# Performance work log

Measured on AMD Instinct MI355X. Metric: run time of the kernel, lower is better.

Reference implementation:

```python
import jax, jax.numpy as jnp
import numpy as np

EPS = 1e-6
STRIDE = 2  # kv_pool_stride
NUM_HEADS = 8

def _layernorm(x, w, b):
    mu = jnp.mean(x, axis=-1, keepdims=True)
    var = jnp.mean(jnp.square(x - mu), axis=-1, keepdims=True)
    return (x - mu) * jax.lax.rsqrt(var + EPS) * w + b

def setup_inputs() -> dict:
    key = jax.random.key(0)
    B, H, W, C = 8, 56, 56, 384
    hidden = int(C * 2.0)
    ks = jax.random.split(key, 12)
    s = 0.02
    return {
        "x": jax.random.normal(ks[0], (B, H * W, C), jnp.float32),
        "ln1_w": jnp.ones((C,), jnp.float32),
        "ln1_b": jnp.zeros((C,), jnp.float32),
        "qw": jax.random.normal(ks[1], (C, C), jnp.float32) * s,
        "qb": jnp.zeros((C,), jnp.float32),
        "kw": jax.random.normal(ks[2], (C, C), jnp.float32) * s,
        "kb": jnp.zeros((C,), jnp.float32),
        "vw": jax.random.normal(ks[3], (C, C), jnp.float32) * s,
        "vb": jnp.zeros((C,), jnp.float32),
        "pw": jax.random.normal(ks[4], (C, C), jnp.float32) * s,
        "pb": jnp.zeros((C,), jnp.float32),
        "ln2_w": jnp.ones((C,), jnp.float32),
        "ln2_b": jnp.zeros((C,), jnp.float32),
        "fc1_w": jax.random.normal(ks[5], (C, hidden), jnp.float32) * s,
        "fc1_b": jnp.zeros((hidden,), jnp.float32),
        "fc2_w": jax.random.normal(ks[6], (hidden, C), jnp.float32) * s,
        "fc2_b": jnp.zeros((C,), jnp.float32),
        "H": 56,
        "W": 56,
    }

def reference(x, ln1_w, ln1_b, qw, qb, kw, kb, vw, vb, pw, pb,
              ln2_w, ln2_b, fc1_w, fc1_b, fc2_w, fc2_b, H, W):
    B, N, C = x.shape
    h = NUM_HEADS
    d = C // h
    scale = d ** -0.5

    # Attention branch: Q from norm1(x); K,V from RAW x (as in source), KV avg-pooled 2x2
    q_tok = _layernorm(x, ln1_w, ln1_b)
    s = STRIDE
    Hk, Wk = H // s, W // s
    kv = x.reshape(B, Hk, s, Wk, s, C).mean(axis=(2, 4)).reshape(B, Hk * Wk, C)

    q = (q_tok @ qw + qb).reshape(B, N, h, d)
    k = (kv @ kw + kb).reshape(B, Hk * Wk, h, d)
    v = (kv @ vw + vb).reshape(B, Hk * Wk, h, d)

    attn = jnp.einsum('bqhd,bkhd->bhqk', q, k) * scale
    attn = jax.nn.softmax(attn, axis=-1)
    out = jnp.einsum('bhqk,bkhd->bqhd', attn, v).reshape(B, N, C)
    x = x + (out @ pw + pb)

    # MLP branch (GELU exact, matching torch nn.GELU default)
    y = _layernorm(x, ln2_w, ln2_b)
    y = jax.nn.gelu(y @ fc1_w + fc1_b, approximate=False)
    x = x + (y @ fc2_w + fc2_b)
    return x
```

## Files before the change

kernel.cpp:

```cpp
#include <hip/hip_runtime.h>
#include <math.h>

#define B_    8
#define N_TOK 3136
#define C_    384
#define DH    48
#define NK    784
#define HID   768
#define M1    25088
#define M2    6272
#define M1Q   6272

typedef unsigned short u16;
typedef __attribute__((ext_vector_type(8))) short bf16x8;
typedef __attribute__((ext_vector_type(4))) float f32x4;

__device__ __forceinline__ float b2f(u16 u) {
  return __uint_as_float(((unsigned)u) << 16);
}
__device__ __forceinline__ u16 f2b(float f) {
  unsigned u = __float_as_uint(f);
  return (u16)((u + 0x7fffu + ((u >> 16) & 1u)) >> 16);
}
__device__ __forceinline__ void gload_lds16(const u16* g, u16* l) {
  __builtin_amdgcn_global_load_lds(
      (const __attribute__((address_space(1))) void*)g,
      (__attribute__((address_space(3))) void*)l, 16, 0, 0);
}
__device__ __forceinline__ unsigned cvtpk_bf16(float a, float b) {
  unsigned r;
  asm("v_cvt_pk_bf16_f32 %0, %1, %2" : "=v"(r) : "v"(a), "v"(b));
  return r;
}
__device__ __forceinline__ float exp2_fast(float x) {
  float r;
  asm("v_exp_f32 %0, %1" : "=v"(r) : "v"(x));
  return r;
}

__global__ __launch_bounds__(256) void ln1_pool(
    const float* __restrict__ X, const float* __restrict__ w,
    const float* __restrict__ b, u16* __restrict__ Y, u16* __restrict__ KV) {
  if (blockIdx.x < M1 / 4) {
    const int row = blockIdx.x * 4 + (threadIdx.x >> 6);
    const int lane = threadIdx.x & 63;
    const size_t base = (size_t)row * C_;
    float v[6];
#pragma unroll
    for (int i = 0; i < 6; ++i) v[i] = X[base + lane + 64 * i];
    float s = 0.f;
#pragma unroll
    for (int i = 0; i < 6; ++i) s += v[i];
#pragma unroll
    for (int off = 32; off > 0; off >>= 1) s += __shfl_xor(s, off);
    const float mu = s * (1.0f / C_);
    float q = 0.f;
#pragma unroll
    for (int i = 0; i < 6; ++i) { float d = v[i] - mu; q += d * d; }
#pragma unroll
    for (int off = 32; off > 0; off >>= 1) q += __shfl_xor(q, off);
    const float r = rsqrtf(q * (1.0f / C_) + 1e-6f);
#pragma unroll
    for (int i = 0; i < 6; ++i) {
      int c = lane + 64 * i;
      Y[base + c] = f2b((v[i] - mu) * r * w[c] + b[c]);
    }
  } else {
    int t = (blockIdx.x - M1 / 4) * 256 + threadIdx.x;
    if (t >= M2 * C_) return;
    int c = t % C_;
    int row = t / C_;
    int bb = row / NK;
    int rr = row - bb * NK;
    int hk = rr / 28;
    int wk = rr - hk * 28;
    const float* p = X + ((size_t)(bb * N_TOK + hk * 112 + wk * 2)) * C_ + c;
    KV[t] = f2b(0.25f * (p[0] + p[C_] + p[56 * C_] + p[57 * C_]));
  }
}

__global__ __launch_bounds__(256) void ln2_rows(const u16* __restrict__ X,
    const float* __restrict__ w, const float* __restrict__ b, u16* __restrict__ Y) {
  const int row = blockIdx.x * 4 + (threadIdx.x >> 6);
  const int lane = threadIdx.x & 63;
  const size_t base = (size_t)row * C_;
  float v[6];
#pragma unroll
  for (int i = 0; i < 6; ++i) v[i] = b2f(X[base + lane + 64 * i]);
  float s = 0.f;
#pragma unroll
  for (int i = 0; i < 6; ++i) s += v[i];
#pragma unroll
  for (int off = 32; off > 0; off >>= 1) s += __shfl_xor(s, off);
  const float mu = s * (1.0f / C_);
  float q = 0.f;
#pragma unroll
  for (int i = 0; i < 6; ++i) { float d = v[i] - mu; q += d * d; }
#pragma unroll
  for (int off = 32; off > 0; off >>= 1) q += __shfl_xor(q, off);
  const float r = rsqrtf(q * (1.0f / C_) + 1e-6f);
#pragma unroll
  for (int i = 0; i < 6; ++i) {
    int c = lane + 64 * i;
    Y[base + c] = f2b((v[i] - mu) * r * w[c] + b[c]);
  }
}

struct TransArgs {
  const float* src[6];
  u16* dst[6];
  int K[6], N[6], tx[6], ty[6];
};
__global__ __launch_bounds__(256) void transpose_all(TransArgs a) {
  const int id = blockIdx.z;
  if ((int)blockIdx.x >= a.tx[id] || (int)blockIdx.y >= a.ty[id]) return;
  const float* W = a.src[id];
  u16* WT = a.dst[id];
  const int K = a.K[id], N = a.N[id];
  __shared__ u16 tile[64][73];
  const int k0 = blockIdx.y * 64, n0 = blockIdx.x * 64;
  for (int i = threadIdx.x; i < 64 * 64; i += 256) {
    int kk = i >> 6, nn = i & 63;
    tile[kk][nn] = f2b(W[(size_t)(k0 + kk) * N + n0 + nn]);
  }
  __syncthreads();
  for (int i = threadIdx.x; i < 64 * 64; i += 256) {
    int nn = i >> 6, kk = i & 63;
    WT[(size_t)(n0 + nn) * K + k0 + kk] = tile[kk][nn];
  }
}

template<int EPI, bool RES32, bool OUT32>
__device__ __forceinline__ void gemm_core(
    const u16* __restrict__ A, const u16* __restrict__ BT,
    const float* __restrict__ bias, const void* __restrict__ resv,
    void* __restrict__ Cv, int N, int K, float oscale, int m0, int n0) {
  __shared__ u16 As[128 * 64];
  __shared__ u16 Bs[128 * 64];
  const int tid  = threadIdx.x;
  const int wave = tid >> 6;
  const int lane = tid & 63;
  const int quad = lane >> 4;
  const int ll   = lane & 15;
  const int wm   = wave >> 1, wn = wave & 1;

  const int srow = wave * 32 + (lane >> 3);
  const int sgs  = lane & 7;

  f32x4 acc[4][4];
#pragma unroll
  for (int i = 0; i < 4; ++i)
#pragma unroll
    for (int j = 0; j < 4; ++j) acc[i][j] = (f32x4){0.f, 0.f, 0.f, 0.f};

  for (int kk0 = 0; kk0 < K; kk0 += 64) {
    __syncthreads();
#pragma unroll
    for (int c = 0; c < 4; ++c) {
      const int r = srow + c * 8;
      const int g = sgs ^ (r & 7);
      gload_lds16(A  + (size_t)(m0 + r) * K + kk0 + g * 8,
                  As + (size_t)(wave * 32 + c * 8) * 64);
      gload_lds16(BT + (size_t)(n0 + r) * K + kk0 + g * 8,
                  Bs + (size_t)(wave * 32 + c * 8) * 64);
    }
    __syncthreads();
#pragma unroll
    for (int ks = 0; ks < 2; ++ks) {
      const int gsw = (quad + 4 * ks) ^ (ll & 7);
      bf16x8 af[4], bfr[4];
#pragma unroll
      for (int im = 0; im < 4; ++im)
        af[im] = *(const bf16x8*)&As[(size_t)(wm * 64 + im * 16 + ll) * 64 + gsw * 8];
#pragma unroll
      for (int jn = 0; jn < 4; ++jn)
        bfr[jn] = *(const bf16x8*)&Bs[(size_t)(wn * 64 + jn * 16 + ll) * 64 + gsw * 8];
#pragma unroll
      for (int im = 0; im < 4; ++im)
#pragma unroll
        for (int jn = 0; jn < 4; ++jn)
          acc[im][jn] = __builtin_amdgcn_mfma_f32_16x16x32_bf16(
              af[im], bfr[jn], acc[im][jn], 0, 0, 0);
    }
  }

  float bb[4];
#pragma unroll
  for (int jn = 0; jn < 4; ++jn) bb[jn] = bias[n0 + wn * 64 + jn * 16 + ll];
#pragma unroll
  for (int im = 0; im < 4; ++im) {
    const int row = m0 + wm * 64 + im * 16 + quad * 4;
#pragma unroll
    for (int jn = 0; jn < 4; ++jn) {
      const int col = n0 + wn * 64 + jn * 16 + ll;
#pragma unroll
      for (int r = 0; r < 4; ++r) {
        float o = (acc[im][jn][r] + bb[jn]) * oscale;
        if (EPI == 1) {
          o = 0.5f * o * (1.0f + erff(o * 0.70710678118654752f));
        } else if (EPI == 2) {
          size_t ri = (size_t)(row + r) * N + col;
          o += RES32 ? ((const float*)resv)[ri] : b2f(((const u16*)resv)[ri]);
        }
        if (OUT32) ((float*)Cv)[(size_t)(row + r) * N + col] = o;
        else       ((u16*)Cv)[(size_t)(row + r) * N + col] = f2b(o);
      }
    }
  }
}

template<int EPI, bool RES32, bool OUT32>
__global__ __launch_bounds__(256) void gemm_bt(
    const u16* __restrict__ A, const u16* __restrict__ BT,
    const float* __restrict__ bias, const void* __restrict__ resv,
    void* __restrict__ Cv, int N, int K) {
  gemm_core<EPI, RES32, OUT32>(A, BT, bias, resv, Cv, N, K, 1.0f,
                               blockIdx.y << 7, blockIdx.x << 7);
}

struct QKVArgs {
  const u16* A[3];
  const u16* BT[3];
  const float* bias[3];
  u16* C[3];
  int M[3];
  float osc[3];
};
__global__ __launch_bounds__(256) void gemm_qkv(QKVArgs a) {
  const int z = blockIdx.z;
  const int m0 = blockIdx.y << 7;
  if (m0 >= a.M[z]) return;
  gemm_core<0, false, false>(a.A[z], a.BT[z], a.bias[z], nullptr, a.C[z],
                             C_, C_, a.osc[z], m0, blockIdx.x << 7);
}

#define QS_STR 72
__global__ __launch_bounds__(512) void attn_mfma(
    const u16* __restrict__ Q, const u16* __restrict__ Kb,
    const u16* __restrict__ Vb, u16* __restrict__ O) {
  __shared__ u16 Ks[2][64 * 64];
  __shared__ u16 Vt[2][48 * QS_STR];
  const int tid  = threadIdx.x;
  const int wave = tid >> 6;
  const int lane = tid & 63;
  const int quad = lane >> 4;
  const int ll   = lane & 15;
  const int blk  = blockIdx.x;
  const int orig = (blk & 7) * 200 + (blk >> 3);
  const int bh   = orig / 25;
  const int qt   = orig - bh * 25;
  const int b    = bh >> 3, h = bh & 7;
  const int q0   = qt * 128;

  bf16x8 qf0, qf1;
  {
    int qrow = q0 + wave * 16 + ll;
    if (qrow >= N_TOK) qrow = N_TOK - 1;
    const u16* qp = Q + ((size_t)(b * N_TOK) + qrow) * C_ + h * DH;
    qf0 = *(const bf16x8*)(qp + quad * 8);
    if (quad < 2) qf1 = *(const bf16x8*)(qp + 32 + quad * 8);
    else          qf1 = (bf16x8){0, 0, 0, 0, 0, 0, 0, 0};
  }

  const int krow = (wave << 3) + (lane >> 3);
  const int kgrp = (lane & 7) ^ (lane >> 3);
  const size_t kbase_g = (size_t)(b * NK) * C_ + h * DH + kgrp * 8;

  uint4 vreg;
  const int vkey  = lane;
  const int vcol  = ((vkey >> 5) << 5) + (((vkey & 15) >> 2) << 3) +
                    (((vkey >> 4) & 1) << 2) + (vkey & 3);

  {
    int kk = krow; if (kk >= NK) kk = NK - 1;
    gload_lds16(Kb + kbase_g + (size_t)kk * C_, &Ks[0][wave << 9]);
    if (wave < 6) {
      int vk = vkey; if (vk >= NK) vk = NK - 1;
      vreg = *(const uint4*)(Vb + ((size_t)(b * NK) + vk) * C_ + h * DH + wave * 8);
      const u16* vp = (const u16*)&vreg;
#pragma unroll
      for (int j = 0; j < 8; ++j)
        Vt[0][(wave * 8 + j) * QS_STR + vcol] = vp[j];
    }
  }
  __syncthreads();

  f32x4 Ofr[3] = {{0.f,0.f,0.f,0.f},{0.f,0.f,0.f,0.f},{0.f,0.f,0.f,0.f}};
  f32x4 Sden = {0.f, 0.f, 0.f, 0.f};
  const short oneb = (short)0x3F80;
  const bf16x8 ones = {oneb, oneb, oneb, oneb, oneb, oneb, oneb, oneb};

  for (int t = 0; t < 13; ++t) {
    const int cur = t & 1, nxt = cur ^ 1;

    if (t < 12) {
      const int knext = (t + 1) * 64;
      int kk = knext + krow; if (kk >= NK) kk = NK - 1;
      gload_lds16(Kb + kbase_g + (size_t)kk * C_, &Ks[nxt][wave << 9]);
      if (wave < 6) {
        int vk = knext + vkey; if (vk >= NK) vk = NK - 1;
        vreg = *(const uint4*)(Vb + ((size_t)(b * NK) + vk) * C_ + h * DH + wave * 8);
      }
    }

    f32x4 S[4];
    __builtin_amdgcn_s_setprio(1);
#pragma unroll
    for (int nt = 0; nt < 4; ++nt) {
      const int rb = (nt * 16 + ll) * 64;
      bf16x8 k0f = *(const bf16x8*)&Ks[cur][rb + ((quad    ) ^ (ll & 7)) * 8];
      bf16x8 k1f = *(const bf16x8*)&Ks[cur][rb + ((quad + 4) ^ (ll & 7)) * 8];
      f32x4 acc = {0.f, 0.f, 0.f, 0.f};
      acc = __builtin_amdgcn_mfma_f32_16x16x32_bf16(k0f, qf0, acc, 0, 0, 0);
      acc = __builtin_amdgcn_mfma_f32_16x16x32_bf16(k1f, qf1, acc, 0, 0, 0);
      S[nt] = acc;
    }
    __builtin_amdgcn_s_setprio(0);

    unsigned pw[8];
    if (t != 12) {
#pragma unroll
      for (int nt = 0; nt < 4; ++nt)
#pragma unroll
        for (int rr = 0; rr < 2; ++rr)
          pw[nt * 2 + rr] =
              cvtpk_bf16(exp2_fast(S[nt][rr * 2]), exp2_fast(S[nt][rr * 2 + 1]));
    } else {
#pragma unroll
      for (int rr = 0; rr < 2; ++rr)
        pw[rr] = cvtpk_bf16(exp2_fast(S[0][rr * 2]), exp2_fast(S[0][rr * 2 + 1]));
#pragma unroll
      for (int i = 2; i < 8; ++i) pw[i] = 0u;
    }
    union PU { unsigned w[4]; bf16x8 v; };
    PU pk0, pk1;
#pragma unroll
    for (int i = 0; i < 4; ++i) { pk0.w[i] = pw[i]; pk1.w[i] = pw[4 + i]; }

    __builtin_amdgcn_s_setprio(1);
    Sden = __builtin_amdgcn_mfma_f32_16x16x32_bf16(pk0.v, ones, Sden, 0, 0, 0);
    Sden = __builtin_amdgcn_mfma_f32_16x16x32_bf16(pk1.v, ones, Sden, 0, 0, 0);

#pragma unroll
    for (int dt = 0; dt < 3; ++dt) {
      bf16x8 v0 = *(const bf16x8*)&Vt[cur][(dt * 16 + ll) * QS_STR + quad * 8];
      bf16x8 v1 = *(const bf16x8*)&Vt[cur][(dt * 16 + ll) * QS_STR + 32 + quad * 8];
      Ofr[dt] = __builtin_amdgcn_mfma_f32_16x16x32_bf16(pk0.v, v0, Ofr[dt], 0, 0, 0);
      Ofr[dt] = __builtin_amdgcn_mfma_f32_16x16x32_bf16(pk1.v, v1, Ofr[dt], 0, 0, 0);
    }
    __builtin_amdgcn_s_setprio(0);

    if (t < 12 && wave < 6) {
      const u16* vp = (const u16*)&vreg;
#pragma unroll
      for (int j = 0; j < 8; ++j)
        Vt[nxt][(wave * 8 + j) * QS_STR + vcol] = vp[j];
    }
    __syncthreads();
  }

  float inv[4];
#pragma unroll
  for (int r = 0; r < 4; ++r) inv[r] = 1.0f / Sden[r];
#pragma unroll
  for (int dt = 0; dt < 3; ++dt)
#pragma unroll
    for (int r = 0; r < 4; ++r) {
      int qrow = q0 + wave * 16 + quad * 4 + r;
      if (qrow < N_TOK)
        O[((size_t)b * N_TOK + qrow) * C_ + h * DH + dt * 16 + ll] =
            f2b(Ofr[dt][r] * inv[r]);
    }
}

__global__ __launch_bounds__(256) void marker_fill(
    float* __restrict__ out, size_t n, float val) {
  size_t i = (size_t)blockIdx.x * 256 + threadIdx.x;
  const size_t stride = (size_t)gridDim.x * 256;
  for (; i < n; i += stride) out[i] = 0.f;
  if (blockIdx.x == 0 && threadIdx.x == 0) out[0] = val;
}

extern "C" void kernel_launch(void* const* d_in, const int* in_sizes, int n_in,
                              void* d_out, int out_size, void* d_ws, size_t ws_size,
                              hipStream_t stream) {
  const float* x    = (const float*)d_in[0];
  const float* ln1w = (const float*)d_in[1];
  const float* ln1b = (const float*)d_in[2];
  const float* qw   = (const float*)d_in[3];
  const float* qb   = (const float*)d_in[4];
  const float* kw   = (const float*)d_in[5];
  const float* kb   = (const float*)d_in[6];
  const float* vw   = (const float*)d_in[7];
  const float* vb   = (const float*)d_in[8];
  const float* pw   = (const float*)d_in[9];
  const float* pb   = (const float*)d_in[10];
  const float* ln2w = (const float*)d_in[11];
  const float* ln2b = (const float*)d_in[12];
  const float* fc1w = (const float*)d_in[13];
  const float* fc1b = (const float*)d_in[14];
  const float* fc2w = (const float*)d_in[15];
  const float* fc2b = (const float*)d_in[16];

  const size_t BUF = (size_t)M1 * C_;
  float* outf = (float*)d_out;

  {
    static const int exp_sizes[19] = {
      M1 * C_, C_, C_, C_ * C_, C_, C_ * C_, C_, C_ * C_, C_, C_ * C_, C_,
      C_, C_, C_ * HID, HID, HID * C_, C_, 1, 1};
    int bad = -1;
    if (n_in != 19) bad = 99;
    else {
      for (int i = 0; i < 19; ++i)
        if (in_sizes[i] != exp_sizes[i]) { bad = i; break; }
    }
    if (bad >= 0) {
      marker_fill<<<1024, 256, 0, stream>>>(outf, BUF, 10000.0f + (float)bad);
      return;
    }
  }
  const size_t need_min  = 4096 + 3 * BUF * sizeof(u16);
  const size_t need_full = 4096 + (3 * BUF + (size_t)M1 * HID) * sizeof(u16);
  if (ws_size < need_min) {
    marker_fill<<<1024, 256, 0, stream>>>(outf, BUF, 30000.0f + (float)(ws_size >> 20));
    return;
  }
  const bool full_mlp = (ws_size >= need_full);

  u16* T0 = (u16*)((char*)d_ws + 4096);
  u16* T1 = T0 + BUF;
  u16* U  = T1 + BUF;
  u16* P  = U;
  u16* KB = U + (size_t)M2 * C_;
  u16* VB = U + (size_t)2 * M2 * C_;
  u16* HBq = U;
  u16* HBfull = U + BUF;
  u16* WTb = U + BUF - (size_t)(4 * C_ * C_ + 2 * C_ * HID);
  u16* wtq = WTb;
  u16* wtk = wtq + C_ * C_;
  u16* wtv = wtk + C_ * C_;
  u16* wtp = wtv + C_ * C_;
  u16* wtf1 = wtp + C_ * C_;
  u16* wtf2 = wtf1 + (size_t)C_ * HID;

  {
    TransArgs ta;
    ta.src[0] = qw;   ta.dst[0] = wtq;  ta.K[0] = C_;  ta.N[0] = C_;  ta.tx[0] = 6;  ta.ty[0] = 6;
    ta.src[1] = kw;   ta.dst[1] = wtk;  ta.K[1] = C_;  ta.N[1] = C_;  ta.tx[1] = 6;  ta.ty[1] = 6;
    ta.src[2] = vw;   ta.dst[2] = wtv;  ta.K[2] = C_;  ta.N[2] = C_;  ta.tx[2] = 6;  ta.ty[2] = 6;
    ta.src[3] = pw;   ta.dst[3] = wtp;  ta.K[3] = C_;  ta.N[3] = C_;  ta.tx[3] = 6;  ta.ty[3] = 6;
    ta.src[4] = fc1w; ta.dst[4] = wtf1; ta.K[4] = C_;  ta.N[4] = HID; ta.tx[4] = 12; ta.ty[4] = 6;
    ta.src[5] = fc2w; ta.dst[5] = wtf2; ta.K[5] = HID; ta.N[5] = C_;  ta.tx[5] = 6;  ta.ty[5] = 12;
    transpose_all<<<dim3(12, 12, 6), 256, 0, stream>>>(ta);
  }

  ln1_pool<<<M1 / 4 + (M2 * C_) / 256, 256, 0, stream>>>(x, ln1w, ln1b, T0, P);

  {
    QKVArgs qa;
    qa.A[0] = T0; qa.BT[0] = wtq; qa.bias[0] = qb; qa.C[0] = T1; qa.M[0] = M1;
    qa.A[1] = P;  qa.BT[1] = wtk; qa.bias[1] = kb; qa.C[1] = KB; qa.M[1] = M2;
    qa.A[2] = P;  qa.BT[2] = wtv; qa.bias[2] = vb; qa.C[2] = VB; qa.M[2] = M2;
    qa.osc[0] = 0.20823509507f;
    qa.osc[1] = 1.0f;
    qa.osc[2] = 1.0f;
    gemm_qkv<<<dim3(3, 196, 3), 256, 0, stream>>>(qa);
  }

  attn_mfma<<<dim3(1600), 512, 0, stream>>>(T1, KB, VB, T0);

  gemm_bt<2, true, false><<<dim3(3, 196), 256, 0, stream>>>(
      T0, wtp, pb, x, T1, C_, C_);

  ln2_rows<<<M1 / 4, 256, 0, stream>>>(T1, ln2w, ln2b, T0);

  if (full_mlp) {
    gemm_bt<1, false, false><<<dim3(6, 196), 256, 0, stream>>>(
        T0, wtf1, fc1b, nullptr, HBfull, HID, C_);
    gemm_bt<2, false, true><<<dim3(3, 196), 256, 0, stream>>>(
        HBfull, wtf2, fc2b, T1, outf, C_, HID);
  } else {
    for (int qtr = 0; qtr < 4; ++qtr) {
      const size_t ro = (size_t)qtr * M1Q;
      gemm_bt<1, false, false><<<dim3(6, 49), 256, 0, stream>>>(
          T0 + ro * C_, wtf1, fc1b, nullptr, HBq, HID, C_);
      gemm_bt<2, false, true><<<dim3(3, 49), 256, 0, stream>>>(
          HBq, wtf2, fc2b, T1 + ro * C_, outf + ro * C_, C_, HID);
    }
  }
}
```

Measured before the change: 312.6 us.

## Fuse projection GEMM with residual add and LayerNorm2; vectorize LN1/pool loads

Replaces the separate projection GEMM and the row LayerNorm kernel with one kernel. Each 512-thread block computes a full 128x384 output tile, adds bias and the residual, writes X1, and reduces row mean and variance through shuffles and LDS so it can emit the normalized bf16 input for fc1. This removes one kernel launch and the re-read of X1, but the launch drops to 196 blocks with heavier per-block work and no double buffering, and variance now uses the E[x^2]-mu^2 form. The LN1 and pooling paths also switch to float2 loads and ushort2 stores.

```diff
diff --git a/kernel.cpp b/kernel.cpp
--- a/kernel.cpp
+++ b/kernel.cpp
@@ -44,65 +44,53 @@
   if (blockIdx.x < M1 / 4) {
     const int row = blockIdx.x * 4 + (threadIdx.x >> 6);
     const int lane = threadIdx.x & 63;
-    const size_t base = (size_t)row * C_;
-    float v[6];
-#pragma unroll
-    for (int i = 0; i < 6; ++i) v[i] = X[base + lane + 64 * i];
+    const float2* xp = (const float2*)(X + (size_t)row * C_);
+    float2 vv[3];
+#pragma unroll
+    for (int i = 0; i < 3; ++i) vv[i] = xp[lane + 64 * i];
     float s = 0.f;
 #pragma unroll
-    for (int i = 0; i < 6; ++i) s += v[i];
+    for (int i = 0; i < 3; ++i) s += vv[i].x + vv[i].y;
 #pragma unroll
     for (int off = 32; off > 0; off >>= 1) s += __shfl_xor(s, off);
     const float mu = s * (1.0f / C_);
     float q = 0.f;
 #pragma unroll
-    for (int i = 0; i < 6; ++i) { float d = v[i] - mu; q += d * d; }
+    for (int i = 0; i < 3; ++i) {
+      float dx = vv[i].x - mu, dy = vv[i].y - mu;
+      q += dx * dx + dy * dy;
+    }
 #pragma unroll
     for (int off = 32; off > 0; off >>= 1) q += __shfl_xor(q, off);
     const float r = rsqrtf(q * (1.0f / C_) + 1e-6f);
-#pragma unroll
-    for (int i = 0; i < 6; ++i) {
-      int c = lane + 64 * i;
-      Y[base + c] = f2b((v[i] - mu) * r * w[c] + b[c]);
+    const float2* wp = (const float2*)w;
+    const float2* bp = (const float2*)b;
+#pragma unroll
+    for (int i = 0; i < 3; ++i) {
+      int cp = lane + 64 * i;
+      float2 wv = wp[cp], bv = bp[cp];
+      u16 o0 = f2b((vv[i].x - mu) * r * wv.x + bv.x);
+      u16 o1 = f2b((vv[i].y - mu) * r * wv.y + bv.y);
+      ushort2 o = {o0, o1};
+      *(ushort2*)&Y[(size_t)row * C_ + cp * 2] = o;
     }
   } else {
     int t = (blockIdx.x - M1 / 4) * 256 + threadIdx.x;
-    if (t >= M2 * C_) return;
-    int c = t % C_;
-    int row = t / C_;
+    if (t >= M2 * (C_ / 2)) return;
+    int cp = t % (C_ / 2);
+    int row = t / (C_ / 2);
     int bb = row / NK;
     int rr = row - bb * NK;
     int hk = rr / 28;
     int wk = rr - hk * 28;
-    const float* p = X + ((size_t)(bb * N_TOK + hk * 112 + wk * 2)) * C_ + c;
-    KV[t] = f2b(0.25f * (p[0] + p[C_] + p[56 * C_] + p[57 * C_]));
-  }
-}
-
-__global__ __launch_bounds__(256) void ln2_rows(const u16* __restrict__ X,
-    const float* __restrict__ w, const float* __restrict__ b, u16* __restrict__ Y) {
-  const int row = blockIdx.x * 4 + (threadIdx.x >> 6);
-  const int lane = threadIdx.x & 63;
-  const size_t base = (size_t)row * C_;
-  float v[6];
-#pragma unroll
-  for (int i = 0; i < 6; ++i) v[i] = b2f(X[base + lane + 64 * i]);
-  float s = 0.f;
-#pragma unroll
-  for (int i = 0; i < 6; ++i) s += v[i];
-#pragma unroll
-  for (int off = 32; off > 0; off >>= 1) s += __shfl_xor(s, off);
-  const float mu = s * (1.0f / C_);
-  float q = 0.f;
-#pragma unroll
-  for (int i = 0; i < 6; ++i) { float d = v[i] - mu; q += d * d; }
-#pragma unroll
-  for (int off = 32; off > 0; off >>= 1) q += __shfl_xor(q, off);
-  const float r = rsqrtf(q * (1.0f / C_) + 1e-6f);
-#pragma unroll
-  for (int i = 0; i < 6; ++i) {
-    int c = lane + 64 * i;
-    Y[base + c] = f2b((v[i] - mu) * r * w[c] + b[c]);
+    const float* p = X + ((size_t)(bb * N_TOK + hk * 112 + wk * 2)) * C_ + cp * 2;
+    float2 a0 = *(const float2*)(p);
+    float2 a1 = *(const float2*)(p + C_);
+    float2 a2 = *(const float2*)(p + 56 * C_);
+    float2 a3 = *(const float2*)(p + 57 * C_);
+    ushort2 o = {f2b(0.25f * (a0.x + a1.x + a2.x + a3.x)),
+                 f2b(0.25f * (a0.y + a1.y + a2.y + a3.y))};
+    *(ushort2*)&KV[(size_t)t * 2] = o;
   }
 }
 
@@ -232,6 +220,147 @@
   if (m0 >= a.M[z]) return;
   gemm_core<0, false, false>(a.A[z], a.BT[z], a.bias[z], nullptr, a.C[z],
                              C_, C_, a.osc[z], m0, blockIdx.x << 7);
+}
+
+__global__ __launch_bounds__(512) void proj_res_ln2(
+    const u16* A, const u16* __restrict__ BT,
+    const float* __restrict__ bias, const float* __restrict__ xres,
+    const float* __restrict__ w2, const float* __restrict__ b2,
+    u16* __restrict__ X1, u16* Y) {
+  __shared__ u16 As[128 * 64];
+  __shared__ u16 Bs[384 * 64];
+  const int tid  = threadIdx.x;
+  const int wave = tid >> 6;
+  const int lane = tid & 63;
+  const int quad = lane >> 4;
+  const int ll   = lane & 15;
+  const int wm   = wave >> 2;
+  const int wn   = wave & 3;
+  const int m0   = blockIdx.x << 7;
+
+  const int srow = tid >> 3;
+  const int g    = (lane & 7) ^ (lane >> 3);
+
+  f32x4 acc[4][6];
+#pragma unroll
+  for (int i = 0; i < 4; ++i)
+#pragma unroll
+    for (int j = 0; j < 6; ++j) acc[i][j] = (f32x4){0.f, 0.f, 0.f, 0.f};
+
+  for (int kk0 = 0; kk0 < 384; kk0 += 64) {
+    __syncthreads();
+#pragma unroll
+    for (int i = 0; i < 8; ++i) {
+      const int row = i * 64 + srow;
+      if (i < 2) {
+        gload_lds16(A + (size_t)(m0 + row) * 384 + kk0 + g * 8,
+                    As + (size_t)(i * 64 + wave * 8) * 64);
+      } else {
+        gload_lds16(BT + (size_t)(row - 128) * 384 + kk0 + g * 8,
+                    Bs + (size_t)((i - 2) * 64 + wave * 8) * 64);
+      }
+    }
+    __syncthreads();
+#pragma unroll
+    for (int ks = 0; ks < 2; ++ks) {
+      const int gsw = (quad + 4 * ks) ^ (ll & 7);
+      bf16x8 af[4], bfr[6];
+#pragma unroll
+      for (int im = 0; im < 4; ++im)
+        af[im] = *(const bf16x8*)&As[(size_t)(wm * 64 + im * 16 + ll) * 64 + gsw * 8];
+#pragma unroll
+      for (int jn = 0; jn < 6; ++jn)
+        bfr[jn] = *(const bf16x8*)&Bs[(size_t)(wn * 96 + jn * 16 + ll) * 64 + gsw * 8];
+#pragma unroll
+      for (int im = 0; im < 4; ++im)
+#pragma unroll
+        for (int jn = 0; jn < 6; ++jn)
+          acc[im][jn] = __builtin_amdgcn_mfma_f32_16x16x32_bf16(
+              af[im], bfr[jn], acc[im][jn], 0, 0, 0);
+    }
+  }
+
+  float bb[6];
+#pragma unroll
+  for (int jn = 0; jn < 6; ++jn) bb[jn] = bias[wn * 96 + jn * 16 + ll];
+  float ps[4][4], pq[4][4];
+#pragma unroll
+  for (int im = 0; im < 4; ++im)
+#pragma unroll
+    for (int r = 0; r < 4; ++r) { ps[im][r] = 0.f; pq[im][r] = 0.f; }
+#pragma unroll
+  for (int im = 0; im < 4; ++im) {
+    const int rid = wm * 64 + im * 16 + quad * 4;
+#pragma unroll
+    for (int jn = 0; jn < 6; ++jn) {
+      const int col = wn * 96 + jn * 16 + ll;
+#pragma unroll
+      for (int r = 0; r < 4; ++r) {
+        float o = acc[im][jn][r] + bb[jn] +
+                  xres[(size_t)(m0 + rid + r) * C_ + col];
+        X1[(size_t)(m0 + rid + r) * C_ + col] = f2b(o);
+        acc[im][jn][r] = o;
+        ps[im][r] += o;
+        pq[im][r] += o * o;
+      }
+    }
+  }
+#pragma unroll
+  for (int msk = 1; msk < 16; msk <<= 1)
+#pragma unroll
+    for (int im = 0; im < 4; ++im)
+#pragma unroll
+      for (int r = 0; r < 4; ++r) {
+        ps[im][r] += __shfl_xor(ps[im][r], msk);
+        pq[im][r] += __shfl_xor(pq[im][r], msk);
+      }
+  __syncthreads();
+  float* pbuf = (float*)As;
+  float* rbm  = pbuf + 128 * 8;
+  if (ll == 0) {
+#pragma unroll
+    for (int im = 0; im < 4; ++im)
+#pragma unroll
+      for (int r = 0; r < 4; ++r) {
+        const int rid = wm * 64 + im * 16 + quad * 4 + r;
+        float2 pr = {ps[im][r], pq[im][r]};
+        *(float2*)&pbuf[rid * 8 + wn * 2] = pr;
+      }
+  }
+  __syncthreads();
+  if (tid < 128) {
+    float s = 0.f, q = 0.f;
+#pragma unroll
+    for (int w = 0; w < 4; ++w) {
+      float2 pr = *(float2*)&pbuf[tid * 8 + w * 2];
+      s += pr.x; q += pr.y;
+    }
+    const float mu  = s * (1.0f / C_);
+    const float var = q * (1.0f / C_) - mu * mu;
+    float2 mr = {mu, rsqrtf(var + 1e-6f)};
+    *(float2*)&rbm[tid * 2] = mr;
+  }
+  __syncthreads();
+  float wc[6], bc[6];
+#pragma unroll
+  for (int jn = 0; jn < 6; ++jn) {
+    const int col = wn * 96 + jn * 16 + ll;
+    wc[jn] = w2[col]; bc[jn] = b2[col];
+  }
+#pragma unroll
+  for (int im = 0; im < 4; ++im) {
+    const int rid = wm * 64 + im * 16 + quad * 4;
+#pragma unroll
+    for (int r = 0; r < 4; ++r) {
+      float2 mr = *(float2*)&rbm[(rid + r) * 2];
+#pragma unroll
+      for (int jn = 0; jn < 6; ++jn) {
+        const int col = wn * 96 + jn * 16 + ll;
+        Y[(size_t)(m0 + rid + r) * C_ + col] =
+            f2b((acc[im][jn][r] - mr.x) * mr.y * wc[jn] + bc[jn]);
+      }
+    }
+  }
 }
 
 #define QS_STR 72
@@ -455,7 +584,8 @@
     transpose_all<<<dim3(12, 12, 6), 256, 0, stream>>>(ta);
   }
 
-  ln1_pool<<<M1 / 4 + (M2 * C_) / 256, 256, 0, stream>>>(x, ln1w, ln1b, T0, P);
+  ln1_pool<<<M1 / 4 + (M2 * (C_ / 2)) / 256, 256, 0, stream>>>(
+      x, ln1w, ln1b, T0, P);
 
   {
     QKVArgs qa;
@@ -470,10 +600,8 @@
 
   attn_mfma<<<dim3(1600), 512, 0, stream>>>(T1, KB, VB, T0);
 
-  gemm_bt<2, true, false><<<dim3(3, 196), 256, 0, stream>>>(
-      T0, wtp, pb, x, T1, C_, C_);
-
-  ln2_rows<<<M1 / 4, 256, 0, stream>>>(T1, ln2w, ln2b, T0);
+  proj_res_ln2<<<dim3(196), 512, 0, stream>>>(
+      T0, wtp, pb, x, ln2w, ln2b, T1, T0);
 
   if (full_mlp) {
     gemm_bt<1, false, false><<<dim3(6, 196), 256, 0, stream>>>(
```

Result: faster. 305.1 us (-2.4%).
